# Kernel optimization log

Measured on AMD Instinct MI355X. Metric: run time of the kernel, lower is better.

Reference implementation:

```python
import jax, jax.numpy as jnp
import numpy as np

D_MODEL = 256

def setup_inputs() -> dict:
    key = jax.random.key(0)
    k_x, k_wqkv, k_bqkv, k_wp, k_bp = jax.random.split(key, 5)
    B, T, d = 4, 4096, D_MODEL
    bound_qkv = 1.0 / np.sqrt(d)
    return {
        "x": jax.random.normal(k_x, (B, T, d), dtype=jnp.float32),
        "W_qkv": jax.random.uniform(k_wqkv, (d, 3 * d), jnp.float32, -bound_qkv, bound_qkv),
        "b_qkv": jax.random.uniform(k_bqkv, (3 * d,), jnp.float32, -bound_qkv, bound_qkv),
        "W_proj": jax.random.uniform(k_wp, (d, d), jnp.float32, -bound_qkv, bound_qkv),
        "b_proj": jax.random.uniform(k_bp, (d,), jnp.float32, -bound_qkv, bound_qkv),
    }

def reference(x, W_qkv, b_qkv, W_proj, b_proj):
    B, T, d = x.shape
    qkv = x @ W_qkv + b_qkv                       # (B, T, 3d)
    q, k, v = jnp.split(qkv, 3, axis=-1)          # each (B, T, d)
    scale = 1.0 / np.sqrt(d).astype(np.float32)
    scores = jnp.einsum('btd,bsd->bts', q, k) * scale   # (B, T, T)
    causal = jnp.tril(jnp.ones((T, T), dtype=bool))     # allowed positions
    scores = jnp.where(causal, scores, -jnp.inf)
    weights = jax.nn.softmax(scores, axis=-1)           # (B, T, T)
    ctx = jnp.einsum('bts,bsd->btd', weights, v)        # (B, T, d)
    return ctx @ W_proj + b_proj
```

## Files before the change

### kernel.cpp

```cpp
#include <hip/hip_runtime.h>
#include <math.h>

#define TT 4096
#define BB 4
#define DM 256
#define NSEG_B 144

typedef __attribute__((ext_vector_type(8))) short short8;
typedef __attribute__((ext_vector_type(4))) short short4v;
typedef __attribute__((ext_vector_type(4))) float f32x4;

#define MFMA16(a, b, c) __builtin_amdgcn_mfma_f32_16x16x32_bf16(a, b, c, 0, 0, 0)

#define GL2LDS(gp, lp) __builtin_amdgcn_global_load_lds( \
    (const __attribute__((address_space(1))) unsigned int*)(gp), \
    (__attribute__((address_space(3))) unsigned int*)(lp), 16, 0, 0)

__device__ __forceinline__ short f2b(float f) {
    union { float f; unsigned u; } v; v.f = f;
    unsigned r = v.u + 0x7FFFu + ((v.u >> 16) & 1u);
    return (short)(r >> 16);
}

__global__ __launch_bounds__(256) void transpose_cast2(
    const float* __restrict__ W1, short* __restrict__ Wt1,
    const float* __restrict__ W2, short* __restrict__ Wt2)
{
    __shared__ float T[64 * 68];
    const int tid = threadIdx.x;
    const int by = blockIdx.y;
    const float* W; short* Wt; int N, n0;
    if (by < 12) { W = W1; Wt = Wt1; N = 768; n0 = by * 64; }
    else         { W = W2; Wt = Wt2; N = 256; n0 = (by - 12) * 64; }
    const int k0 = blockIdx.x * 64;
#pragma unroll
    for (int it = 0; it < 4; ++it) {
        int idx = tid + it * 256;
        int r = idx >> 4, c4 = idx & 15;
        *(float4*)&T[r * 68 + c4 * 4] =
            *(const float4*)&W[(size_t)(k0 + r) * N + n0 + c4 * 4];
    }
    __syncthreads();
#pragma unroll
    for (int it = 0; it < 4; ++it) {
        int idx = tid + it * 256;
        int n = idx >> 4, c4 = idx & 15;
        short4v t;
#pragma unroll
        for (int j = 0; j < 4; ++j) t[j] = f2b(T[(c4 * 4 + j) * 68 + n]);
        *(short4v*)&Wt[(size_t)(n0 + n) * 256 + k0 + c4 * 4] = t;
    }
}

__global__ __launch_bounds__(256) void qkv_gemm(
    const float* __restrict__ x, const short* __restrict__ Bt,
    const float* __restrict__ bias, short* __restrict__ qkvb,
    short* __restrict__ VtG)
{
    __shared__ short As[16384];
    __shared__ short Bs[16384];
    __shared__ short Ts[64 * 72];

    const int tid = threadIdx.x;
    const int w = tid >> 6, lane = tid & 63;
    const int l15 = lane & 15, quad = lane >> 4;
    const int m0 = blockIdx.x * 64;
    const int nsup = blockIdx.y * 384;

#pragma unroll
    for (int it = 0; it < 8; ++it) {
        int idx = tid + it * 256;
        int row = ((idx >> 9) << 4) + (idx & 15);
        int col = ((idx >> 6) & 7) * 32 + ((idx >> 4) & 3) * 8;
        const float* src = &x[(size_t)(m0 + row) * 256 + col];
        float4 u = *(const float4*)src, u2 = *(const float4*)(src + 4);
        short8 t;
        t[0] = f2b(u.x);  t[1] = f2b(u.y);  t[2] = f2b(u.z);  t[3] = f2b(u.w);
        t[4] = f2b(u2.x); t[5] = f2b(u2.y); t[6] = f2b(u2.z); t[7] = f2b(u2.w);
        *(short8*)&As[idx * 8] = t;
    }

    for (int t6 = 0; t6 < 6; ++t6) {
        const int n0 = nsup + t6 * 64;
#pragma unroll
        for (int it = 0; it < 8; ++it) {
            int idx = tid + it * 256;
            int n = ((idx >> 9) << 4) + (idx & 15);
            int col = ((idx >> 6) & 7) * 32 + ((idx >> 4) & 3) * 8;
            *(short8*)&Bs[idx * 8] = *(const short8*)&Bt[(size_t)(n0 + n) * 256 + col];
        }
        __syncthreads();

        f32x4 acc[4];
#pragma unroll
        for (int t = 0; t < 4; ++t) acc[t] = (f32x4){0.f, 0.f, 0.f, 0.f};
#pragma unroll
        for (int k0 = 0; k0 < 8; ++k0) {
            short8 a = *(const short8*)&As[((w * 8 + k0) * 64 + lane) * 8];
#pragma unroll
            for (int nt = 0; nt < 4; ++nt) {
                short8 bb = *(const short8*)&Bs[((nt * 8 + k0) * 64 + lane) * 8];
                acc[nt] = MFMA16(a, bb, acc[nt]);
            }
        }

        if (n0 < 512) {
#pragma unroll
            for (int nt = 0; nt < 4; ++nt) {
                int n = n0 + nt * 16 + l15;
                float bv = bias[n];
#pragma unroll
                for (int r = 0; r < 4; ++r)
                    qkvb[(size_t)(m0 + w * 16 + quad * 4 + r) * 768 + n]
                        = f2b(acc[nt][r] + bv);
            }
            __syncthreads();
        } else {
#pragma unroll
            for (int nt = 0; nt < 4; ++nt) {
                int n = n0 + nt * 16 + l15;
                float bv = bias[n];
#pragma unroll
                for (int r = 0; r < 4; ++r)
                    Ts[(nt * 16 + l15) * 72 + w * 16 + quad * 4 + r]
                        = f2b(acc[nt][r] + bv);
            }
            __syncthreads();
            const int d  = tid >> 2;
            const int c  = tid & 3;
            short8 v0 = *(const short8*)&Ts[d * 72 + c * 16];
            short8 v1 = *(const short8*)&Ts[d * 72 + c * 16 + 8];
            const int bg = m0 >> 12, key0 = (m0 & 4095) + c * 16;
            short* dst = &VtG[((size_t)bg * 256 + (n0 - 512) + d) * 4096 + key0];
            *(short8*)dst = v0;
            *(short8*)(dst + 8) = v1;
        }
    }
}

__global__ __launch_bounds__(256, 2) void flash_mfma(
    const short* __restrict__ qkv,
    const short* __restrict__ VtG,
    float* __restrict__ Opart,
    float* __restrict__ L)
{
    __shared__ short Ks[2][4096];
    __shared__ short Vs[2][8192];
    __shared__ short Ps[4096];

    const int tid = threadIdx.x;
    const int w = tid >> 6, lane = tid & 63;
    const int l15 = lane & 15, quad = lane >> 4;

    const int b = blockIdx.x & 3;
    const int e = (NSEG_B - 1) - (blockIdx.x >> 2);
    const int lid = b * NSEG_B + e;
    int g = 0;
    while (g < 7 && e >= 2 * (g + 1) * (g + 2)) ++g;
    int off = e - 2 * g * (g + 1);
    int qt = 4 * g + off / (g + 1);
    int s  = off - (off / (g + 1)) * (g + 1);
    const int kp_lo = s * 16;
    const int kp_hi = min(kp_lo + 16, 4 * (qt + 1));
    const int npairs = kp_hi - kp_lo;

    const size_t base = (size_t)b * TT * 768;
    const int row0 = qt * 128;

    short8 aq[2][8];
#pragma unroll
    for (int rs = 0; rs < 2; ++rs) {
        const short* qrow = &qkv[base + (size_t)(row0 + rs * 64 + w * 16 + l15) * 768 + quad * 8];
#pragma unroll
        for (int k0 = 0; k0 < 8; ++k0)
            aq[rs][k0] = *(const short8*)&qrow[k0 * 32];
    }

#pragma unroll
    for (int it = 0; it < 2; ++it) {
        int idx = tid + it * 256;
        int row = idx & 15;
        int col = ((idx >> 6) & 7) * 32 + ((idx >> 4) & 3) * 8;
        GL2LDS(&qkv[base + (size_t)(kp_lo * 32 + row) * 768 + 256 + col], &Ks[0][idx * 8]);
    }
    __builtin_amdgcn_sched_barrier(0);
#pragma unroll
    for (int it = 0; it < 4; ++it) {
        int idx = tid + it * 256;
        int d  = ((idx >> 6) << 4) + (idx & 15);
        int kc = ((idx >> 4) & 3) * 8;
        GL2LDS(&VtG[((size_t)b * 256 + d) * 4096 + kp_lo * 32 + kc], &Vs[0][idx * 8]);
    }

    f32x4 o[2][16];
#pragma unroll
    for (int rs = 0; rs < 2; ++rs)
#pragma unroll
        for (int c = 0; c < 16; ++c) o[rs][c] = (f32x4){0.f, 0.f, 0.f, 0.f};
    float l_acc[2][4] = {{0.f, 0.f, 0.f, 0.f}, {0.f, 0.f, 0.f, 0.f}};

    for (int u = 0; u < npairs; ++u) {
        const int j0 = (kp_lo + u) * 32;

        __syncthreads();

#pragma unroll
        for (int it = 0; it < 2; ++it) {
            int idx = tid + it * 256;
            int row = idx & 15;
            int col = ((idx >> 6) & 7) * 32 + ((idx >> 4) & 3) * 8;
            GL2LDS(&qkv[base + (size_t)(j0 + 16 + row) * 768 + 256 + col], &Ks[1][idx * 8]);
        }
        __builtin_amdgcn_sched_barrier(0);
        if (u + 1 < npairs) {
#pragma unroll
            for (int it = 0; it < 4; ++it) {
                int idx = tid + it * 256;
                int d  = ((idx >> 6) << 4) + (idx & 15);
                int kc = ((idx >> 4) & 3) * 8;
                GL2LDS(&VtG[((size_t)b * 256 + d) * 4096 + j0 + 32 + kc],
                       &Vs[(u + 1) & 1][idx * 8]);
            }
        }
        __builtin_amdgcn_sched_barrier(0);

        {
            f32x4 s4[2];
            s4[0] = (f32x4){0.f, 0.f, 0.f, 0.f};
            s4[1] = (f32x4){0.f, 0.f, 0.f, 0.f};
#pragma unroll
            for (int k0 = 0; k0 < 8; ++k0) {
                short8 bb = *(const short8*)&Ks[0][(k0 * 64 + lane) * 8];
                s4[0] = MFMA16(aq[0][k0], bb, s4[0]);
                s4[1] = MFMA16(aq[1][k0], bb, s4[1]);
            }
#pragma unroll
            for (int rs = 0; rs < 2; ++rs)
#pragma unroll
                for (int r = 0; r < 4; ++r) {
                    const int rg = row0 + rs * 64 + w * 16 + quad * 4 + r;
                    int jg = j0 + l15;
                    float xx = s4[rs][r] * 0.0625f;
                    if (jg > rg) xx = -INFINITY;
                    float pv = __expf(fminf(xx, 30.f));
                    l_acc[rs][r] += pv;
                    Ps[((rs * 4 + w) * 64 + (0 * 2 + (l15 >> 3)) * 16 + quad * 4 + r) * 8
                       + (l15 & 7)] = f2b(pv);
                }
        }

        if (u + 1 < npairs) {
            asm volatile("s_waitcnt vmcnt(4)" ::: "memory");
        } else {
            asm volatile("s_waitcnt vmcnt(0)" ::: "memory");
        }
        __builtin_amdgcn_s_barrier();
        __builtin_amdgcn_sched_barrier(0);

        if (u + 1 < npairs) {
#pragma unroll
            for (int it = 0; it < 2; ++it) {
                int idx = tid + it * 256;
                int row = idx & 15;
                int col = ((idx >> 6) & 7) * 32 + ((idx >> 4) & 3) * 8;
                GL2LDS(&qkv[base + (size_t)(j0 + 32 + row) * 768 + 256 + col], &Ks[0][idx * 8]);
            }
        }
        __builtin_amdgcn_sched_barrier(0);

        {
            f32x4 s4[2];
            s4[0] = (f32x4){0.f, 0.f, 0.f, 0.f};
            s4[1] = (f32x4){0.f, 0.f, 0.f, 0.f};
#pragma unroll
            for (int k0 = 0; k0 < 8; ++k0) {
                short8 bb = *(const short8*)&Ks[1][(k0 * 64 + lane) * 8];
                s4[0] = MFMA16(aq[0][k0], bb, s4[0]);
                s4[1] = MFMA16(aq[1][k0], bb, s4[1]);
            }
#pragma unroll
            for (int rs = 0; rs < 2; ++rs)
#pragma unroll
                for (int r = 0; r < 4; ++r) {
                    const int rg = row0 + rs * 64 + w * 16 + quad * 4 + r;
                    int jg = j0 + 16 + l15;
                    float xx = s4[rs][r] * 0.0625f;
                    if (jg > rg) xx = -INFINITY;
                    float pv = __expf(fminf(xx, 30.f));
                    l_acc[rs][r] += pv;
                    Ps[((rs * 4 + w) * 64 + (1 * 2 + (l15 >> 3)) * 16 + quad * 4 + r) * 8
                       + (l15 & 7)] = f2b(pv);
                }
        }

        {
            short8 a0 = *(const short8*)&Ps[((0 * 4 + w) * 64 + lane) * 8];
            short8 a1 = *(const short8*)&Ps[((1 * 4 + w) * 64 + lane) * 8];
#pragma unroll
            for (int ct = 0; ct < 16; ++ct) {
                short8 bb = *(const short8*)&Vs[u & 1][(ct * 64 + lane) * 8];
                o[0][ct] = MFMA16(a0, bb, o[0][ct]);
                o[1][ct] = MFMA16(a1, bb, o[1][ct]);
            }
        }
    }

#pragma unroll
    for (int rs = 0; rs < 2; ++rs)
#pragma unroll
        for (int r = 0; r < 4; ++r) {
            float l = l_acc[rs][r];
            l += __shfl_xor(l, 1); l += __shfl_xor(l, 2);
            l += __shfl_xor(l, 4); l += __shfl_xor(l, 8);
            if (l15 == 0)
                L[(size_t)lid * 128 + rs * 64 + w * 16 + quad * 4 + r] = l;
        }
    const size_t ob = (size_t)lid * (128 * 256);
#pragma unroll
    for (int rs = 0; rs < 2; ++rs)
#pragma unroll
        for (int r = 0; r < 4; ++r) {
            int lr = rs * 64 + w * 16 + quad * 4 + r;
#pragma unroll
            for (int c = 0; c < 16; ++c)
                Opart[ob + (size_t)lr * 256 + c * 16 + l15] = o[rs][c][r];
        }
}

__global__ __launch_bounds__(256) void proj_gemm(
    const float* __restrict__ Opart, const float* __restrict__ L,
    const short* __restrict__ Bt, const float* __restrict__ bias,
    float* __restrict__ out)
{
    __shared__ short As[16384];
    __shared__ short Bs[16384];
    __shared__ float Linv[64];

    const int tid = threadIdx.x;
    const int w = tid >> 6, lane = tid & 63;
    const int l15 = lane & 15, quad = lane >> 4;
    const int t = blockIdx.x;
    const int b = t >> 6, q64 = t & 63;
    const int qt = q64 >> 1, half = q64 & 1;
    const int gg = qt >> 2, rr = qt & 3;
    const int sbase = b * NSEG_B + 2 * gg * (gg + 1) + rr * (gg + 1);
    const int nseg = gg + 1;
    const int m0 = t * 64;
    const int ro = half * 64;

    if (tid < 64) {
        float l = 0.f;
#pragma unroll
        for (int s2 = 0; s2 < 8; ++s2)
            if (s2 < nseg) l += L[(size_t)(sbase + s2) * 128 + ro + tid];
        Linv[tid] = 1.f / l;
    }
    __syncthreads();

#pragma unroll
    for (int it = 0; it < 8; ++it) {
        int idx = tid + it * 256;
        int row = ((idx >> 9) << 4) + (idx & 15);
        int col = ((idx >> 6) & 7) * 32 + ((idx >> 4) & 3) * 8;
        float a8[8] = {0.f, 0.f, 0.f, 0.f, 0.f, 0.f, 0.f, 0.f};
#pragma unroll
        for (int s2 = 0; s2 < 8; ++s2) {
            if (s2 < nseg) {
                const float* src = &Opart[(size_t)(sbase + s2) * 32768
                                          + (size_t)(ro + row) * 256 + col];
                float4 u = *(const float4*)src, u2 = *(const float4*)(src + 4);
                a8[0] += u.x;  a8[1] += u.y;  a8[2] += u.z;  a8[3] += u.w;
                a8[4] += u2.x; a8[5] += u2.y; a8[6] += u2.z; a8[7] += u2.w;
            }
        }
        float inv = Linv[row];
        short8 t8;
#pragma unroll
        for (int j = 0; j < 8; ++j) t8[j] = f2b(a8[j] * inv);
        *(short8*)&As[idx * 8] = t8;
    }

    for (int t2 = 0; t2 < 4; ++t2) {
        const int n0 = t2 * 64;
#pragma unroll
        for (int it = 0; it < 8; ++it) {
            int idx = tid + it * 256;
            int n = ((idx >> 9) << 4) + (idx & 15);
            int col = ((idx >> 6) & 7) * 32 + ((idx >> 4) & 3) * 8;
            *(short8*)&Bs[idx * 8] = *(const short8*)&Bt[(size_t)(n0 + n) * 256 + col];
        }
        __syncthreads();

        f32x4 acc[4];
#pragma unroll
        for (int tt = 0; tt < 4; ++tt) acc[tt] = (f32x4){0.f, 0.f, 0.f, 0.f};
#pragma unroll
        for (int k0 = 0; k0 < 8; ++k0) {
            short8 a = *(const short8*)&As[((w * 8 + k0) * 64 + lane) * 8];
#pragma unroll
            for (int nt = 0; nt < 4; ++nt) {
                short8 bb = *(const short8*)&Bs[((nt * 8 + k0) * 64 + lane) * 8];
                acc[nt] = MFMA16(a, bb, acc[nt]);
            }
        }
#pragma unroll
        for (int nt = 0; nt < 4; ++nt) {
            int n = n0 + nt * 16 + l15;
            float bv = bias[n];
#pragma unroll
            for (int r = 0; r < 4; ++r)
                out[(size_t)(m0 + w * 16 + quad * 4 + r) * 256 + n] = acc[nt][r] + bv;
        }
        __syncthreads();
    }
}

extern "C" void kernel_launch(void* const* d_in, const int* in_sizes, int n_in,
                              void* d_out, int out_size, void* d_ws, size_t ws_size,
                              hipStream_t stream)
{
    const float* x     = (const float*)d_in[0];
    const float* Wqkv  = (const float*)d_in[1];
    const float* bqkv  = (const float*)d_in[2];
    const float* Wproj = (const float*)d_in[3];
    const float* bproj = (const float*)d_in[4];
    float* out = (float*)d_out;

    const size_t M = (size_t)BB * TT;
    short* qkv_b = (short*)d_ws;
    short* Wt1   = qkv_b + M * 768;
    short* Wt2   = Wt1 + (size_t)768 * 256;
    short* VtG   = Wt2 + (size_t)256 * 256;
    float* Opart = (float*)(VtG + (size_t)BB * 256 * 4096);
    float* L     = Opart + (size_t)BB * NSEG_B * 128 * 256;

    dim3 blk(256);
    transpose_cast2<<<dim3(4, 16), blk, 0, stream>>>(Wqkv, Wt1, Wproj, Wt2);
    qkv_gemm<<<dim3(256, 2), blk, 0, stream>>>(x, Wt1, bqkv, qkv_b, VtG);
    flash_mfma<<<dim3(BB * NSEG_B), blk, 0, stream>>>(qkv_b, VtG, Opart, L);
    proj_gemm<<<dim3(256), blk, 0, stream>>>(Opart, L, Wt2, bproj, out);
}
```

Baseline: 239.1 us.

## Single-buffer V tile in flash kernel and halve proj_gemm row tile

The flash kernel drops the double-buffered V tile in LDS. V is now loaded once per iteration into a single buffer and waited on just before the PV MFMAs, which cuts LDS use and may allow more resident blocks, but exposes more V load latency. Separately, proj_gemm now processes 32 rows per block instead of 64 and launches 512 blocks, with the four waves split across M and N. This raises parallelism in the output projection and shrinks its LDS footprint.

```diff
diff --git a/kernel.cpp b/kernel.cpp
--- a/kernel.cpp
+++ b/kernel.cpp
@@ -145,7 +145,7 @@
     float* __restrict__ L)
 {
     __shared__ short Ks[2][4096];
-    __shared__ short Vs[2][8192];
+    __shared__ short Vs[8192];
     __shared__ short Ps[4096];
 
     const int tid = threadIdx.x;
@@ -183,14 +183,6 @@
         int col = ((idx >> 6) & 7) * 32 + ((idx >> 4) & 3) * 8;
         GL2LDS(&qkv[base + (size_t)(kp_lo * 32 + row) * 768 + 256 + col], &Ks[0][idx * 8]);
     }
-    __builtin_amdgcn_sched_barrier(0);
-#pragma unroll
-    for (int it = 0; it < 4; ++it) {
-        int idx = tid + it * 256;
-        int d  = ((idx >> 6) << 4) + (idx & 15);
-        int kc = ((idx >> 4) & 3) * 8;
-        GL2LDS(&VtG[((size_t)b * 256 + d) * 4096 + kp_lo * 32 + kc], &Vs[0][idx * 8]);
-    }
 
     f32x4 o[2][16];
 #pragma unroll
@@ -212,15 +204,12 @@
             GL2LDS(&qkv[base + (size_t)(j0 + 16 + row) * 768 + 256 + col], &Ks[1][idx * 8]);
         }
         __builtin_amdgcn_sched_barrier(0);
-        if (u + 1 < npairs) {
-#pragma unroll
-            for (int it = 0; it < 4; ++it) {
-                int idx = tid + it * 256;
-                int d  = ((idx >> 6) << 4) + (idx & 15);
-                int kc = ((idx >> 4) & 3) * 8;
-                GL2LDS(&VtG[((size_t)b * 256 + d) * 4096 + j0 + 32 + kc],
-                       &Vs[(u + 1) & 1][idx * 8]);
-            }
+#pragma unroll
+        for (int it = 0; it < 4; ++it) {
+            int idx = tid + it * 256;
+            int d  = ((idx >> 6) << 4) + (idx & 15);
+            int kc = ((idx >> 4) & 3) * 8;
+            GL2LDS(&VtG[((size_t)b * 256 + d) * 4096 + j0 + kc], &Vs[idx * 8]);
         }
         __builtin_amdgcn_sched_barrier(0);
 
@@ -249,11 +238,7 @@
                 }
         }
 
-        if (u + 1 < npairs) {
-            asm volatile("s_waitcnt vmcnt(4)" ::: "memory");
-        } else {
-            asm volatile("s_waitcnt vmcnt(0)" ::: "memory");
-        }
+        asm volatile("s_waitcnt vmcnt(4)" ::: "memory");
         __builtin_amdgcn_s_barrier();
         __builtin_amdgcn_sched_barrier(0);
 
@@ -293,12 +278,20 @@
                 }
         }
 
+        if (u + 1 < npairs) {
+            asm volatile("s_waitcnt vmcnt(2)" ::: "memory");
+        } else {
+            asm volatile("s_waitcnt vmcnt(0)" ::: "memory");
+        }
+        __builtin_amdgcn_s_barrier();
+        __builtin_amdgcn_sched_barrier(0);
+
         {
             short8 a0 = *(const short8*)&Ps[((0 * 4 + w) * 64 + lane) * 8];
             short8 a1 = *(const short8*)&Ps[((1 * 4 + w) * 64 + lane) * 8];
 #pragma unroll
             for (int ct = 0; ct < 16; ++ct) {
-                short8 bb = *(const short8*)&Vs[u & 1][(ct * 64 + lane) * 8];
+                short8 bb = *(const short8*)&Vs[(ct * 64 + lane) * 8];
                 o[0][ct] = MFMA16(a0, bb, o[0][ct]);
                 o[1][ct] = MFMA16(a1, bb, o[1][ct]);
             }
@@ -332,23 +325,23 @@
     const short* __restrict__ Bt, const float* __restrict__ bias,
     float* __restrict__ out)
 {
-    __shared__ short As[16384];
+    __shared__ short As[8192];
     __shared__ short Bs[16384];
-    __shared__ float Linv[64];
+    __shared__ float Linv[32];
 
     const int tid = threadIdx.x;
     const int w = tid >> 6, lane = tid & 63;
     const int l15 = lane & 15, quad = lane >> 4;
     const int t = blockIdx.x;
-    const int b = t >> 6, q64 = t & 63;
-    const int qt = q64 >> 1, half = q64 & 1;
+    const int b = t >> 7, q32 = t & 127;
+    const int qt = q32 >> 2;
+    const int ro = (q32 & 3) * 32;
     const int gg = qt >> 2, rr = qt & 3;
     const int sbase = b * NSEG_B + 2 * gg * (gg + 1) + rr * (gg + 1);
     const int nseg = gg + 1;
-    const int m0 = t * 64;
-    const int ro = half * 64;
-
-    if (tid < 64) {
+    const int m0 = t * 32;
+
+    if (tid < 32) {
         float l = 0.f;
 #pragma unroll
         for (int s2 = 0; s2 < 8; ++s2)
@@ -358,7 +351,7 @@
     __syncthreads();
 
 #pragma unroll
-    for (int it = 0; it < 8; ++it) {
+    for (int it = 0; it < 4; ++it) {
         int idx = tid + it * 256;
         int row = ((idx >> 9) << 4) + (idx & 15);
         int col = ((idx >> 6) & 7) * 32 + ((idx >> 4) & 3) * 8;
@@ -391,25 +384,26 @@
         }
         __syncthreads();
 
-        f32x4 acc[4];
-#pragma unroll
-        for (int tt = 0; tt < 4; ++tt) acc[tt] = (f32x4){0.f, 0.f, 0.f, 0.f};
+        f32x4 acc[2];
+        acc[0] = (f32x4){0.f, 0.f, 0.f, 0.f};
+        acc[1] = (f32x4){0.f, 0.f, 0.f, 0.f};
 #pragma unroll
         for (int k0 = 0; k0 < 8; ++k0) {
-            short8 a = *(const short8*)&As[((w * 8 + k0) * 64 + lane) * 8];
-#pragma unroll
-            for (int nt = 0; nt < 4; ++nt) {
-                short8 bb = *(const short8*)&Bs[((nt * 8 + k0) * 64 + lane) * 8];
+            short8 a = *(const short8*)&As[(((w & 1) * 8 + k0) * 64 + lane) * 8];
+#pragma unroll
+            for (int nt = 0; nt < 2; ++nt) {
+                int n16 = (w >> 1) * 2 + nt;
+                short8 bb = *(const short8*)&Bs[((n16 * 8 + k0) * 64 + lane) * 8];
                 acc[nt] = MFMA16(a, bb, acc[nt]);
             }
         }
 #pragma unroll
-        for (int nt = 0; nt < 4; ++nt) {
-            int n = n0 + nt * 16 + l15;
+        for (int nt = 0; nt < 2; ++nt) {
+            int n = n0 + ((w >> 1) * 2 + nt) * 16 + l15;
             float bv = bias[n];
 #pragma unroll
             for (int r = 0; r < 4; ++r)
-                out[(size_t)(m0 + w * 16 + quad * 4 + r) * 256 + n] = acc[nt][r] + bv;
+                out[(size_t)(m0 + (w & 1) * 16 + quad * 4 + r) * 256 + n] = acc[nt][r] + bv;
         }
         __syncthreads();
     }
@@ -434,9 +428,8 @@
     float* Opart = (float*)(VtG + (size_t)BB * 256 * 4096);
     float* L     = Opart + (size_t)BB * NSEG_B * 128 * 256;
 
-    dim3 blk(256);
-    transpose_cast2<<<dim3(4, 16), blk, 0, stream>>>(Wqkv, Wt1, Wproj, Wt2);
-    qkv_gemm<<<dim3(256, 2), blk, 0, stream>>>(x, Wt1, bqkv, qkv_b, VtG);
-    flash_mfma<<<dim3(BB * NSEG_B), blk, 0, stream>>>(qkv_b, VtG, Opart, L);
-    proj_gemm<<<dim3(256), blk, 0, stream>>>(Opart, L, Wt2, bproj, out);
-}
+    transpose_cast2<<<dim3(4, 16), dim3(256), 0, stream>>>(Wqkv, Wt1, Wproj, Wt2);
+    qkv_gemm<<<dim3(256, 2), dim3(256), 0, stream>>>(x, Wt1, bqkv, qkv_b, VtG);
+    flash_mfma<<<dim3(BB * NSEG_B), dim3(256), 0, stream>>>(qkv_b, VtG, Opart, L);
+    proj_gemm<<<dim3(512), dim3(256), 0, stream>>>(Opart, L, Wt2, bproj, out);
+}
```

Measured after the change: 212.1 us. 11.3% less time.
